# Performance work log

Hardware: AMD Instinct MI355X
Metric: run time of the kernel (lower is better)

The kernel has to match this reference:

```python
import jax, jax.numpy as jnp
import numpy as np
from jax import lax

D_MODEL, D_STATE, D_CONV, EXPAND = 64, 16, 4, 2
D_INNER = EXPAND * D_MODEL          # 128
DT_RANK = (D_MODEL + 15) // 16      # 4 = ceil(d_model/16), mamba_ssm 'auto'
B, L, N_IDX = 512, 256, 2048


def setup_inputs() -> dict:
    key = jax.random.key(0)
    ks = jax.random.split(key, 14)
    g = lambda k, shape, s: jax.random.normal(k, shape, jnp.float32) * s
    return {
        "reads": jax.random.normal(ks[0], (B, L, 4), jnp.float32),
        "sequenced_reads_indices": jax.random.randint(ks[1], (N_IDX,), 0, B),
        "exp_w": g(ks[2], (4, D_MODEL), 0.5),
        "exp_b": jnp.zeros((D_MODEL,), jnp.float32),
        "in_proj_w": g(ks[3], (D_MODEL, 2 * D_INNER), 0.1),
        "conv_w": g(ks[4], (D_INNER, 1, D_CONV), 0.3),
        "conv_b": jnp.zeros((D_INNER,), jnp.float32),
        "x_proj_w": g(ks[5], (D_INNER, DT_RANK + 2 * D_STATE), 0.1),
        "dt_w": g(ks[6], (DT_RANK, D_INNER), 0.3),
        "dt_b": jnp.full((D_INNER,), -4.6, jnp.float32),  # softplus(-4.6) ~ 0.01, mamba dt init scale
        "A_log": jnp.log(jnp.broadcast_to(jnp.arange(1, D_STATE + 1, dtype=jnp.float32), (D_INNER, D_STATE))),
        "D_skip": jnp.ones((D_INNER,), jnp.float32),
        "out_proj_w": g(ks[7], (D_INNER, D_MODEL), 0.1),
        "q_w": g(ks[8], (2 * D_MODEL, D_MODEL), 0.1),
        "q_b": jnp.zeros((D_MODEL,), jnp.float32),
        "k_w": g(ks[9], (2 * D_MODEL, D_MODEL), 0.1),
        "k_b": jnp.zeros((D_MODEL,), jnp.float32),
    }


def _mamba(x, in_proj_w, conv_w, conv_b, x_proj_w, dt_w, dt_b, A_log, D_skip, out_proj_w):
    # x: [b, l, d_model]
    xm, z = jnp.split(x @ in_proj_w, 2, axis=-1)  # each [b, l, d_inner]
    # causal depthwise conv over the sequence axis (pad left by d_conv-1, truncate to l)
    xc = lax.conv_general_dilated(
        xm.transpose(0, 2, 1), conv_w, (1,), [(D_CONV - 1, 0)],
        dimension_numbers=("NCH", "OIH", "NCH"), feature_group_count=D_INNER)
    xc = jax.nn.silu(xc + conv_b[None, :, None]).transpose(0, 2, 1)  # [b, l, d_inner]
    dt, Bm, Cm = jnp.split(xc @ x_proj_w, [DT_RANK, DT_RANK + D_STATE], axis=-1)
    delta = jax.nn.softplus(dt @ dt_w + dt_b)  # [b, l, d_inner]
    A = -jnp.exp(A_log)                        # [d_inner, d_state]

    def step(h, inp):
        d_t, B_t, C_t, u_t = inp  # [b,di], [b,ds], [b,ds], [b,di]
        h = jnp.exp(d_t[:, :, None] * A) * h + (d_t * u_t)[:, :, None] * B_t[:, None, :]
        return h, jnp.einsum("bdn,bn->bd", h, C_t)

    h0 = jnp.zeros((x.shape[0], D_INNER, D_STATE), x.dtype)
    xs = (delta.transpose(1, 0, 2), Bm.transpose(1, 0, 2),
          Cm.transpose(1, 0, 2), xc.transpose(1, 0, 2))
    _, ys = lax.scan(jax.checkpoint(step), h0, xs)  # ys: [l, b, d_inner]
    y = ys.transpose(1, 0, 2) + xc * D_skip
    return (y * jax.nn.silu(z)) @ out_proj_w  # [b, l, d_model]


def reference(reads, sequenced_reads_indices, exp_w, exp_b, in_proj_w, conv_w, conv_b,
              x_proj_w, dt_w, dt_b, A_log, D_skip, out_proj_w, q_w, q_b, k_w, k_b):
    x = reads @ exp_w + exp_b  # [b, l, d_model]
    enc = _mamba(x, in_proj_w, conv_w, conv_b, x_proj_w, dt_w, dt_b, A_log, D_skip, out_proj_w)
    mean_pooled = enc.mean(axis=1)        # [b, d_model]
    last_pooled = enc[:, -1, :]           # [b, d_model] (max pool computed in torch but unused)
    pooled = jnp.concatenate([mean_pooled, last_pooled], axis=-1)  # [b, 2*d_model]
    seq = pooled[sequenced_reads_indices]  # [n, 2*d_model]
    queries = seq @ q_w + q_b
    keys = pooled @ k_w + k_b
    return jnp.einsum("nd,md->nm", queries, keys)  # [n, b]
```

## Files before the change

### kernel.cpp

```cpp
#include <hip/hip_runtime.h>
#include <math.h>

#define L_SEQ 256
#define TILE 32

typedef __attribute__((ext_vector_type(2))) float f32x2;
typedef __attribute__((ext_vector_type(4))) float f32x4;
typedef __attribute__((ext_vector_type(8))) _Float16 f16x8;
typedef __attribute__((ext_vector_type(2))) _Float16 f16x2;

__device__ __forceinline__ f32x2 fma2(f32x2 a, f32x2 b, f32x2 c) {
    return __builtin_elementwise_fma(a, b, c);
}
__device__ __forceinline__ f32x2 splat2(float x) { f32x2 v = {x, x}; return v; }
__device__ __forceinline__ float silu_f(float x) { return x / (1.f + __expf(-x)); }
__device__ __forceinline__ float sp2_f(float x) {
    return log2f(1.f + exp2f(x * 1.44269504f)) * 0.69314718f;
}

__global__ __launch_bounds__(256)
void k_prep1(const float* __restrict__ exp_w, const float* __restrict__ exp_b,
             const float* __restrict__ in_proj_w,
             float* __restrict__ weff, float* __restrict__ beff)
{
    const int t = threadIdx.x;
    float a0 = 0, a1 = 0, a2 = 0, a3 = 0, ab = 0;
    for (int k = 0; k < 64; ++k) {
        float w = in_proj_w[k * 256 + t];
        a0 = fmaf(exp_w[k], w, a0);
        a1 = fmaf(exp_w[64 + k], w, a1);
        a2 = fmaf(exp_w[128 + k], w, a2);
        a3 = fmaf(exp_w[192 + k], w, a3);
        ab = fmaf(exp_b[k], w, ab);
    }
    weff[t] = a0; weff[256 + t] = a1; weff[512 + t] = a2; weff[768 + t] = a3;
    beff[t] = ab;
}

__global__ __launch_bounds__(256)
void k_prep2(const float* __restrict__ x_proj_w, const float* __restrict__ dt_w,
             const float* __restrict__ conv_w, const float* __restrict__ conv_b,
             const float* __restrict__ weff, const float* __restrict__ beff,
             _Float16* __restrict__ WT, _Float16* __restrict__ W2, float* __restrict__ bias2)
{
    const int t = threadIdx.x;
    const int blk = blockIdx.x;
    if (blk < 5) {
        const int base = blk * 4096;
        for (int i = base + t; i < base + 4096; i += 256) {
            const int row = i >> 7, k = i & 127;
            float v;
            if (row < 128) {
                v = x_proj_w[k * 36 + 0] * dt_w[row]
                  + x_proj_w[k * 36 + 1] * dt_w[128 + row]
                  + x_proj_w[k * 36 + 2] * dt_w[256 + row]
                  + x_proj_w[k * 36 + 3] * dt_w[384 + row];
            } else {
                v = x_proj_w[k * 36 + 4 + (row - 128)];
            }
            WT[i] = (_Float16)v;
        }
    } else if (blk == 5) {
        for (int i = t; i < 128 * 32; i += 256) {
            const int d = i >> 5, j = i & 31;
            float v = 0.f;
            if (j < 16)      v = conv_w[d * 4 + (j >> 2)] * weff[(j & 3) * 256 + d];
            else if (j < 20) v = conv_w[d * 4 + (j - 16)] * beff[d];
            W2[i] = (_Float16)v;
        }
        if (t < 128) bias2[t] = conv_b[t];
    } else {
        for (int i = t; i < 128 * 32; i += 256) {
            const int d = i >> 5, j = i & 31;
            float v = 0.f;
            if (j >= 12 && j < 16) v = weff[(j - 12) * 256 + 128 + d];
            else if (j == 19)      v = beff[128 + d];
            W2[128 * 32 + i] = (_Float16)v;
        }
    }
}

template<int NSEG>
__global__ __launch_bounds__(512, 6)
void mamba_seg(const float* __restrict__ reads,
               const _Float16* __restrict__ WT, const _Float16* __restrict__ W2,
               const float* __restrict__ bias2, const float* __restrict__ dt_b,
               const float* __restrict__ A_log, const float* __restrict__ D_skip,
               f16x2* __restrict__ Qg, f16x2* __restrict__ Pg, f16x2* __restrict__ Kg,
               float* __restrict__ GS, float* __restrict__ CZ, float* __restrict__ SL,
               int Bn)
{
    constexpr int NTILE_ = (L_SEQ / TILE) / NSEG;
    const int bx = blockIdx.x;
    const int b = bx / NSEG;
    const int sidx = bx - b * NSEG;
    const int seg0 = sidx * NTILE_ * TILE;
    const int t = threadIdx.x;
    const int dd = t >> 1, g = t & 1;

    __shared__ __align__(16) _Float16 F[32 * 40];
    __shared__ __align__(16) _Float16 XC[TILE * 136];
    __shared__ __align__(16) float    BC[TILE * 32];
    __shared__ _Float16               ZS[TILE * 128];
    __shared__ _Float16               DE[TILE * 128];

    float dskip = 0.f, c1 = 0.f;
    bool structured = true;
    if (t < 256) {
        dskip = D_skip[dd];
        c1 = -1.44269504f * (float)(8 * g + 1);
#pragma unroll
        for (int k = 0; k < 8; ++k) {
            float a = -__expf(A_log[dd * 16 + g * 8 + k]);
            structured = structured && (fabsf(a + (float)(g * 8 + k + 1)) < 1e-3f);
        }
    }

    f32x2 h2[4], P2[4], K2[4];
#pragma unroll
    for (int k = 0; k < 4; ++k) { h2[k] = splat2(0.f); P2[k] = splat2(1.f); K2[k] = splat2(0.f); }
    float gsum = 0.f;

    for (int tile = 0; tile < NTILE_; ++tile) {
        const int l_off = seg0 + tile * TILE;

        for (int i = t; i < 32 * 40; i += 512) {
            const int l = i / 40, j = i - l * 40;
            _Float16 v = (_Float16)0.f;
            if (j < 16) {
                const int row = l_off + l - 3 + (j >> 2);
                if (row >= 0) v = (_Float16)reads[((size_t)b * L_SEQ + row) * 4 + (j & 3)];
            } else if (j < 20) {
                v = (l_off + l - 3 + (j - 16) >= 0) ? (_Float16)1.f : (_Float16)0.f;
            }
            F[i] = v;
        }
        __syncthreads();

        {
            const int lane = t & 63, wv = t >> 6;
            const int fcol = lane & 15, kq = lane >> 4, rbase = kq * 4;
#pragma unroll
            for (int i = 0; i < 4; ++i) {
                const int tid = wv + 8 * i;
                const int m = tid & 1, n = tid >> 1;
                f16x8 af = *(const f16x8*)&F[(m * 16 + fcol) * 40 + kq * 8];
                f16x8 bf = *(const f16x8*)&W2[(n * 16 + fcol) * 32 + kq * 8];
                f32x4 acc = {0.f, 0.f, 0.f, 0.f};
                acc = __builtin_amdgcn_mfma_f32_16x16x32_f16(af, bf, acc, 0, 0, 0);
                if (n < 8) {
                    const int ch = n * 16 + fcol;
                    const float bv = bias2[ch];
#pragma unroll
                    for (int r = 0; r < 4; ++r)
                        XC[(m * 16 + rbase + r) * 136 + ch] = (_Float16)silu_f(acc[r] + bv);
                } else {
                    const int ch = (n - 8) * 16 + fcol;
#pragma unroll
                    for (int r = 0; r < 4; ++r)
                        ZS[(m * 16 + rbase + r) * 128 + ch] = (_Float16)silu_f(acc[r]);
                }
            }
        }
        __syncthreads();

        {
            const int lane = t & 63, wv = t >> 6;
            const int fcol = lane & 15, kq = lane >> 4, rbase = kq * 4;
#pragma unroll
            for (int i = 0; i < 3; ++i) {
                const int tid = wv + 8 * i;
                if (tid >= 20) break;
                const int m = tid & 1, n = tid >> 1;
                f32x4 acc = {0.f, 0.f, 0.f, 0.f};
#pragma unroll
                for (int ks = 0; ks < 4; ++ks) {
                    const int ko = ks * 32 + kq * 8;
                    f16x8 af = *(const f16x8*)&XC[(m * 16 + fcol) * 136 + ko];
                    f16x8 bf = *(const f16x8*)&WT[(n * 16 + fcol) * 128 + ko];
                    acc = __builtin_amdgcn_mfma_f32_16x16x32_f16(af, bf, acc, 0, 0, 0);
                }
                if (n < 8) {
                    const int ch = n * 16 + fcol;
                    const float db = dt_b[ch];
#pragma unroll
                    for (int r = 0; r < 4; ++r)
                        DE[(m * 16 + rbase + r) * 128 + ch] = (_Float16)sp2_f(acc[r] + db);
                } else {
                    const int jb = (n - 8) * 16 + fcol;
#pragma unroll
                    for (int r = 0; r < 4; ++r)
                        BC[(m * 16 + rbase + r) * 32 + jb] = acc[r];
                }
            }
        }
        __syncthreads();

        if (t < 256) {
            auto scan_loop = [&](bool needpk) {
                for (int l = 0; l < TILE; ++l) {
                    const float de = (float)DE[l * 128 + dd];
                    const float zs = (float)ZS[l * 128 + dd];
                    const float xc = (float)XC[l * 136 + dd];
                    const float du = de * xc;
                    f32x2 E2[4];
                    if (structured) {
                        const float r = exp2f(de * -1.44269504f);
                        const float t1 = exp2f(de * c1);
                        const float r2 = r * r;
                        E2[0] = (f32x2){t1, t1 * r};
                        const f32x2 r2s = splat2(r2);
                        E2[1] = E2[0] * r2s;
                        E2[2] = E2[1] * r2s;
                        E2[3] = E2[2] * r2s;
                    } else {
#pragma unroll
                        for (int k = 0; k < 4; ++k) {
                            float e0 = exp2f(de * (-__expf(A_log[dd * 16 + g * 8 + 2 * k])) * 1.44269504f);
                            float e1 = exp2f(de * (-__expf(A_log[dd * 16 + g * 8 + 2 * k + 1])) * 1.44269504f);
                            E2[k] = (f32x2){e0, e1};
                        }
                    }
                    const float4 Bq0 = *(const float4*)&BC[l * 32 + g * 8];
                    const float4 Bq1 = *(const float4*)&BC[l * 32 + g * 8 + 4];
                    const float4 Cq0 = *(const float4*)&BC[l * 32 + 16 + g * 8];
                    const float4 Cq1 = *(const float4*)&BC[l * 32 + 16 + g * 8 + 4];
                    const f32x2 B2[4] = {{Bq0.x, Bq0.y}, {Bq0.z, Bq0.w}, {Bq1.x, Bq1.y}, {Bq1.z, Bq1.w}};
                    const f32x2 C2[4] = {{Cq0.x, Cq0.y}, {Cq0.z, Cq0.w}, {Cq1.x, Cq1.y}, {Cq1.z, Cq1.w}};
                    const f32x2 dus = splat2(du), zss = splat2(zs);
                    f32x2 yp2 = splat2(0.f);
#pragma unroll
                    for (int k = 0; k < 4; ++k) {
                        h2[k] = fma2(E2[k], h2[k], dus * B2[k]);
                        yp2 = fma2(h2[k], C2[k], yp2);
                        if (needpk) {
                            P2[k] = P2[k] * E2[k];
                            K2[k] = fma2(zss, C2[k] * P2[k], K2[k]);
                        }
                    }
                    float yp = yp2.x + yp2.y;
                    const float y = yp + __shfl_xor(yp, 1);
                    gsum += fmaf(xc, dskip, y) * zs;
                }
            };
            if (sidx == 0) scan_loop(false);
            else           scan_loop(true);
        }
        if (NTILE_ > 1) __syncthreads();
    }

    if (t < 256) {
        const float zs_last = (float)ZS[(TILE - 1) * 128 + dd];
        const float xc_last = (float)XC[(TILE - 1) * 136 + dd];
        const size_t sb = (size_t)sidx * Bn + b;
#pragma unroll
        for (int k = 0; k < 4; ++k) {
            const size_t o = (sb * 8 + g * 4 + k) * 128 + dd;
            Qg[o] = (f16x2){(_Float16)h2[k].x, (_Float16)h2[k].y};
            if (sidx != 0) {
                Pg[o] = (f16x2){(_Float16)P2[k].x, (_Float16)P2[k].y};
                Kg[o] = (f16x2){(_Float16)K2[k].x, (_Float16)K2[k].y};
            }
        }
        if (g == 0) GS[sb * 128 + dd] = gsum;
        if (sidx == NSEG - 1) {
#pragma unroll
            for (int k = 0; k < 8; ++k)
                CZ[((size_t)b * 16 + g * 8 + k) * 128 + dd] =
                    zs_last * BC[(TILE - 1) * 32 + 16 + g * 8 + k];
            if (g == 0) SL[(size_t)b * 128 + dd] = zs_last * xc_last * dskip;
        }
    }
}

template<int NS>
__global__ __launch_bounds__(128)
void stitch(const f16x2* __restrict__ Qg, const f16x2* __restrict__ Pg,
            const f16x2* __restrict__ Kg, const float* __restrict__ GS,
            const float* __restrict__ CZ, const float* __restrict__ SL,
            const float* __restrict__ out_proj_w,
            const float* __restrict__ k_w, const float* __restrict__ k_b,
            float* __restrict__ pooled, float* __restrict__ keysT,
            int Bn)
{
    const int b = blockIdx.x, d = threadIdx.x;
    __shared__ float gb[256];
    __shared__ float pl[128];

    float h[16];
    float gsum = GS[(size_t)b * 128 + d];
#pragma unroll
    for (int p = 0; p < 8; ++p) {
        f16x2 q = Qg[((size_t)b * 8 + p) * 128 + d];
        h[2 * p] = (float)q[0]; h[2 * p + 1] = (float)q[1];
    }
#pragma unroll
    for (int s = 1; s < NS; ++s) {
        const size_t sb = (size_t)s * Bn + b;
        gsum += GS[sb * 128 + d];
        float corr = 0.f;
#pragma unroll
        for (int p = 0; p < 8; ++p) {
            const size_t o = (sb * 8 + p) * 128 + d;
            f16x2 qv = Qg[o], pv = Pg[o], kv = Kg[o];
            corr = fmaf((float)kv[0], h[2 * p], corr);
            corr = fmaf((float)kv[1], h[2 * p + 1], corr);
            h[2 * p]     = fmaf((float)pv[0], h[2 * p],     (float)qv[0]);
            h[2 * p + 1] = fmaf((float)pv[1], h[2 * p + 1], (float)qv[1]);
        }
        gsum += corr;
    }
    float glast = SL[(size_t)b * 128 + d];
#pragma unroll
    for (int n = 0; n < 16; ++n)
        glast = fmaf(CZ[((size_t)b * 16 + n) * 128 + d], h[n], glast);

    gb[d] = gsum * (1.f / (float)L_SEQ);
    gb[128 + d] = glast;
    __syncthreads();
    {
        const int half = d >> 6, oc = d & 63;
        const float* gbp = &gb[half * 128];
        float s = 0.f;
#pragma unroll 16
        for (int i = 0; i < 128; ++i) s = fmaf(gbp[i], out_proj_w[i * 64 + oc], s);
        pooled[(size_t)b * 128 + d] = s;
        pl[d] = s;
    }
    __syncthreads();
    if (d < 64) {
        float s = k_b[d];
#pragma unroll 16
        for (int i = 0; i < 128; ++i) s = fmaf(pl[i], k_w[i * 64 + d], s);
        keysT[(size_t)d * Bn + b] = s;
    }
}

__global__ __launch_bounds__(128)
void qk_kernel(const float* __restrict__ pooled, const int* __restrict__ idx,
               const float* __restrict__ q_w, const float* __restrict__ q_b,
               const float* __restrict__ keysT, float* __restrict__ out, int B)
{
    const int n = blockIdx.x, t = threadIdx.x;
    __shared__ float p_lds[128];
    __shared__ float q_lds[64];
    const int bi = idx[n];
    p_lds[t] = pooled[(size_t)bi * 128 + t];
    __syncthreads();
    if (t < 64) {
        float s = q_b[t];
#pragma unroll
        for (int i = 0; i < 128; ++i) s = fmaf(p_lds[i], q_w[i * 64 + t], s);
        q_lds[t] = s;
    }
    __syncthreads();
    f32x4 acc = {0.f, 0.f, 0.f, 0.f};
    const int m0 = t * 4;
#pragma unroll 8
    for (int i = 0; i < 64; ++i) {
        const float qi = q_lds[i];
        const float4 kv = *(const float4*)&keysT[(size_t)i * B + m0];
        acc[0] = fmaf(qi, kv.x, acc[0]);
        acc[1] = fmaf(qi, kv.y, acc[1]);
        acc[2] = fmaf(qi, kv.z, acc[2]);
        acc[3] = fmaf(qi, kv.w, acc[3]);
    }
    *(f32x4*)&out[(size_t)n * B + m0] = acc;
}


extern "C" void kernel_launch(void* const* d_in, const int* in_sizes, int n_in,
                              void* d_out, int out_size, void* d_ws, size_t ws_size,
                              hipStream_t stream)
{
    const float* reads      = (const float*)d_in[0];
    const int*   idx        = (const int*)d_in[1];
    const float* exp_w      = (const float*)d_in[2];
    const float* exp_b      = (const float*)d_in[3];
    const float* in_proj_w  = (const float*)d_in[4];
    const float* conv_w     = (const float*)d_in[5];
    const float* conv_b     = (const float*)d_in[6];
    const float* x_proj_w   = (const float*)d_in[7];
    const float* dt_w       = (const float*)d_in[8];
    const float* dt_b       = (const float*)d_in[9];
    const float* A_log      = (const float*)d_in[10];
    const float* D_skip     = (const float*)d_in[11];
    const float* out_proj_w = (const float*)d_in[12];
    const float* q_w        = (const float*)d_in[13];
    const float* q_b        = (const float*)d_in[14];
    const float* k_w        = (const float*)d_in[15];
    const float* k_b        = (const float*)d_in[16];

    const int B = in_sizes[0] / (L_SEQ * 4);
    const int N = in_sizes[1];

    char* wsb = (char*)d_ws;
    size_t off = 0;
    auto alloc = [&](size_t bytes) {
        size_t o = off;
        off = (off + bytes + 255) & ~(size_t)255;
        return o;
    };

    float*     pooled = (float*)(wsb + alloc((size_t)B * 128 * 4));
    float*     keysT  = (float*)(wsb + alloc((size_t)B * 64 * 4));
    float*     weff   = (float*)(wsb + alloc(1024 * 4));
    float*     beff   = (float*)(wsb + alloc(256 * 4));
    _Float16*  WT     = (_Float16*)(wsb + alloc(160 * 128 * 2));
    _Float16*  W2     = (_Float16*)(wsb + alloc(256 * 32 * 2));
    float*     bias2  = (float*)(wsb + alloc(128 * 4));

    auto summ_bytes = [&](int nseg) {
        size_t pairs = (size_t)B * nseg * 8 * 128;
        return pairs * 4 * 3
             + (size_t)B * nseg * 128 * 4
             + (size_t)B * 16 * 128 * 4
             + (size_t)B * 128 * 4 + 8192;
    };
    const int nseg = (off + summ_bytes(8) <= ws_size) ? 8 : 1;

    const size_t pairs = (size_t)B * nseg * 8 * 128;
    f16x2* Qg = (f16x2*)(wsb + alloc(pairs * 4));
    f16x2* Pg = (f16x2*)(wsb + alloc(pairs * 4));
    f16x2* Kg = (f16x2*)(wsb + alloc(pairs * 4));
    float* GS = (float*)(wsb + alloc((size_t)B * nseg * 128 * 4));
    float* CZ = (float*)(wsb + alloc((size_t)B * 16 * 128 * 4));
    float* SL = (float*)(wsb + alloc((size_t)B * 128 * 4));

    k_prep1<<<1, 256, 0, stream>>>(exp_w, exp_b, in_proj_w, weff, beff);
    k_prep2<<<7, 256, 0, stream>>>(x_proj_w, dt_w, conv_w, conv_b, weff, beff,
                                   WT, W2, bias2);
    if (nseg == 8) {
        mamba_seg<8><<<B * 8, 512, 0, stream>>>(reads, WT, W2, bias2, dt_b,
                                                A_log, D_skip,
                                                Qg, Pg, Kg, GS, CZ, SL, B);
        stitch<8><<<B, 128, 0, stream>>>(Qg, Pg, Kg, GS, CZ, SL, out_proj_w, k_w, k_b,
                                         pooled, keysT, B);
    } else {
        mamba_seg<1><<<B, 512, 0, stream>>>(reads, WT, W2, bias2, dt_b,
                                            A_log, D_skip,
                                            Qg, Pg, Kg, GS, CZ, SL, B);
        stitch<1><<<B, 128, 0, stream>>>(Qg, Pg, Kg, GS, CZ, SL, out_proj_w, k_w, k_b,
                                         pooled, keysT, B);
    }
    qk_kernel<<<N, 128, 0, stream>>>(pooled, idx, q_w, q_b, keysT, (float*)d_out, B);
}
```

Baseline: 140.9 us.

## Fuse prep kernels, run two scan segments per block, pack summaries, pair qk rows

Merges the two weight-prep kernels into one launch. Restructures the Mamba segment kernel so each 512-thread block handles two 32-step segments, with both 256-thread halves running scans instead of half the threads idling during the scan phase. The per-segment Q/P/K summaries are packed into one 16-byte f16x8 record, reducing separate loads in the stitch pass at the cost of some padding bytes. The qk kernel now computes two query rows per block to reuse key loads. This also removes the fallback to single-segment mode when workspace is small.

```diff
diff --git a/kernel.cpp b/kernel.cpp
--- a/kernel.cpp
+++ b/kernel.cpp
@@ -3,11 +3,11 @@
 
 #define L_SEQ 256
 #define TILE 32
+#define NSEG 8
 
 typedef __attribute__((ext_vector_type(2))) float f32x2;
 typedef __attribute__((ext_vector_type(4))) float f32x4;
 typedef __attribute__((ext_vector_type(8))) _Float16 f16x8;
-typedef __attribute__((ext_vector_type(2))) _Float16 f16x2;
 
 __device__ __forceinline__ f32x2 fma2(f32x2 a, f32x2 b, f32x2 c) {
     return __builtin_elementwise_fma(a, b, c);
@@ -19,32 +19,13 @@
 }
 
 __global__ __launch_bounds__(256)
-void k_prep1(const float* __restrict__ exp_w, const float* __restrict__ exp_b,
-             const float* __restrict__ in_proj_w,
-             float* __restrict__ weff, float* __restrict__ beff)
+void k_prep(const float* __restrict__ exp_w, const float* __restrict__ exp_b,
+            const float* __restrict__ in_proj_w, const float* __restrict__ x_proj_w,
+            const float* __restrict__ dt_w,
+            const float* __restrict__ conv_w, const float* __restrict__ conv_b,
+            _Float16* __restrict__ WT, _Float16* __restrict__ W2, float* __restrict__ bias2)
 {
-    const int t = threadIdx.x;
-    float a0 = 0, a1 = 0, a2 = 0, a3 = 0, ab = 0;
-    for (int k = 0; k < 64; ++k) {
-        float w = in_proj_w[k * 256 + t];
-        a0 = fmaf(exp_w[k], w, a0);
-        a1 = fmaf(exp_w[64 + k], w, a1);
-        a2 = fmaf(exp_w[128 + k], w, a2);
-        a3 = fmaf(exp_w[192 + k], w, a3);
-        ab = fmaf(exp_b[k], w, ab);
-    }
-    weff[t] = a0; weff[256 + t] = a1; weff[512 + t] = a2; weff[768 + t] = a3;
-    beff[t] = ab;
-}
-
-__global__ __launch_bounds__(256)
-void k_prep2(const float* __restrict__ x_proj_w, const float* __restrict__ dt_w,
-             const float* __restrict__ conv_w, const float* __restrict__ conv_b,
-             const float* __restrict__ weff, const float* __restrict__ beff,
-             _Float16* __restrict__ WT, _Float16* __restrict__ W2, float* __restrict__ bias2)
-{
-    const int t = threadIdx.x;
-    const int blk = blockIdx.x;
+    const int t = threadIdx.x, blk = blockIdx.x;
     if (blk < 5) {
         const int base = blk * 4096;
         for (int i = base + t; i < base + 4096; i += 256) {
@@ -60,214 +41,217 @@
             }
             WT[i] = (_Float16)v;
         }
-    } else if (blk == 5) {
-        for (int i = t; i < 128 * 32; i += 256) {
-            const int d = i >> 5, j = i & 31;
-            float v = 0.f;
-            if (j < 16)      v = conv_w[d * 4 + (j >> 2)] * weff[(j & 3) * 256 + d];
-            else if (j < 20) v = conv_w[d * 4 + (j - 16)] * beff[d];
-            W2[i] = (_Float16)v;
-        }
-        if (t < 128) bias2[t] = conv_b[t];
     } else {
-        for (int i = t; i < 128 * 32; i += 256) {
-            const int d = i >> 5, j = i & 31;
-            float v = 0.f;
-            if (j >= 12 && j < 16) v = weff[(j - 12) * 256 + 128 + d];
-            else if (j == 19)      v = beff[128 + d];
-            W2[128 * 32 + i] = (_Float16)v;
-        }
-    }
-}
-
-template<int NSEG>
-__global__ __launch_bounds__(512, 6)
-void mamba_seg(const float* __restrict__ reads,
-               const _Float16* __restrict__ WT, const _Float16* __restrict__ W2,
-               const float* __restrict__ bias2, const float* __restrict__ dt_b,
-               const float* __restrict__ A_log, const float* __restrict__ D_skip,
-               f16x2* __restrict__ Qg, f16x2* __restrict__ Pg, f16x2* __restrict__ Kg,
-               float* __restrict__ GS, float* __restrict__ CZ, float* __restrict__ SL,
-               int Bn)
+        const int d = t & 127;
+        const int col = (t < 128) ? d : (128 + d);
+        float w0 = 0, w1 = 0, w2 = 0, w3 = 0, bb = 0;
+        for (int k = 0; k < 64; ++k) {
+            float w = in_proj_w[k * 256 + col];
+            w0 = fmaf(exp_w[k], w, w0);
+            w1 = fmaf(exp_w[64 + k], w, w1);
+            w2 = fmaf(exp_w[128 + k], w, w2);
+            w3 = fmaf(exp_w[192 + k], w, w3);
+            bb = fmaf(exp_b[k], w, bb);
+        }
+        const float wx[4] = {w0, w1, w2, w3};
+        if (t < 128) {
+            for (int j = 0; j < 32; ++j) {
+                float v = 0.f;
+                if (j < 16)      v = conv_w[d * 4 + (j >> 2)] * wx[j & 3];
+                else if (j < 20) v = conv_w[d * 4 + (j - 16)] * bb;
+                W2[d * 32 + j] = (_Float16)v;
+            }
+            bias2[d] = conv_b[d];
+        } else {
+            for (int j = 0; j < 32; ++j) {
+                float v = 0.f;
+                if (j >= 12 && j < 16) v = wx[j - 12];
+                else if (j == 19)      v = bb;
+                W2[(128 + d) * 32 + j] = (_Float16)v;
+            }
+        }
+    }
+}
+
+__global__ __launch_bounds__(512, 2)
+void mamba_seg2(const float* __restrict__ reads,
+                const _Float16* __restrict__ WT, const _Float16* __restrict__ W2,
+                const float* __restrict__ bias2, const float* __restrict__ dt_b,
+                const float* __restrict__ A_log, const float* __restrict__ D_skip,
+                f16x8* __restrict__ QPK, float* __restrict__ GS,
+                float* __restrict__ CZ, float* __restrict__ SL, int Bn)
 {
-    constexpr int NTILE_ = (L_SEQ / TILE) / NSEG;
     const int bx = blockIdx.x;
-    const int b = bx / NSEG;
-    const int sidx = bx - b * NSEG;
-    const int seg0 = sidx * NTILE_ * TILE;
+    const int b = bx >> 2, jp = bx & 3;
     const int t = threadIdx.x;
-    const int dd = t >> 1, g = t & 1;
-
-    __shared__ __align__(16) _Float16 F[32 * 40];
-    __shared__ __align__(16) _Float16 XC[TILE * 136];
-    __shared__ __align__(16) float    BC[TILE * 32];
-    __shared__ _Float16               ZS[TILE * 128];
-    __shared__ _Float16               DE[TILE * 128];
-
-    float dskip = 0.f, c1 = 0.f;
+    const int lane256 = t & 255, wg = t >> 8;
+    const int dd = lane256 >> 1, g = lane256 & 1;
+    const int sidx = jp * 2 + wg;
+
+    __shared__ __align__(16) _Float16 F2[2][32 * 40];
+    __shared__ __align__(16) _Float16 XC2[2][32 * 136];
+    __shared__ __align__(16) float    BC2[2][32 * 32];
+    __shared__ _Float16               ZS2[2][32 * 128];
+    __shared__ _Float16               DE2[2][32 * 128];
+
+    const float dskip = D_skip[dd];
+    const float c1 = -1.44269504f * (float)(8 * g + 1);
     bool structured = true;
-    if (t < 256) {
-        dskip = D_skip[dd];
-        c1 = -1.44269504f * (float)(8 * g + 1);
-#pragma unroll
-        for (int k = 0; k < 8; ++k) {
-            float a = -__expf(A_log[dd * 16 + g * 8 + k]);
-            structured = structured && (fabsf(a + (float)(g * 8 + k + 1)) < 1e-3f);
-        }
-    }
+#pragma unroll
+    for (int k = 0; k < 8; ++k) {
+        float a = -__expf(A_log[dd * 16 + g * 8 + k]);
+        structured = structured && (fabsf(a + (float)(g * 8 + k + 1)) < 1e-3f);
+    }
+
+    for (int i = t; i < 2 * 32 * 40; i += 512) {
+        const int tau = i / 1280, r = i - tau * 1280;
+        const int l = r / 40, j = r - l * 40;
+        const int l_off = jp * 64 + tau * 32;
+        _Float16 v = (_Float16)0.f;
+        if (j < 16) {
+            const int row = l_off + l - 3 + (j >> 2);
+            if (row >= 0) v = (_Float16)reads[((size_t)b * L_SEQ + row) * 4 + (j & 3)];
+        } else if (j < 20) {
+            v = (l_off + l - 3 + (j - 16) >= 0) ? (_Float16)1.f : (_Float16)0.f;
+        }
+        F2[0][i] = v;
+    }
+    __syncthreads();
+
+    const int lane = t & 63, wv = t >> 6;
+    const int fcol = lane & 15, kq = lane >> 4, rbase = kq * 4;
+
+#pragma unroll
+    for (int i = 0; i < 8; ++i) {
+        const int tt = wv + 8 * i;
+        const int tau = tt >> 5, tid = tt & 31;
+        const int m = tid & 1, n = tid >> 1;
+        f16x8 af = *(const f16x8*)&F2[tau][(m * 16 + fcol) * 40 + kq * 8];
+        f16x8 bf = *(const f16x8*)&W2[(n * 16 + fcol) * 32 + kq * 8];
+        f32x4 acc = {0.f, 0.f, 0.f, 0.f};
+        acc = __builtin_amdgcn_mfma_f32_16x16x32_f16(af, bf, acc, 0, 0, 0);
+        if (n < 8) {
+            const int ch = n * 16 + fcol;
+            const float bv = bias2[ch];
+#pragma unroll
+            for (int r = 0; r < 4; ++r)
+                XC2[tau][(m * 16 + rbase + r) * 136 + ch] = (_Float16)silu_f(acc[r] + bv);
+        } else {
+            const int ch = (n - 8) * 16 + fcol;
+#pragma unroll
+            for (int r = 0; r < 4; ++r)
+                ZS2[tau][(m * 16 + rbase + r) * 128 + ch] = (_Float16)silu_f(acc[r]);
+        }
+    }
+    __syncthreads();
+
+#pragma unroll
+    for (int i = 0; i < 5; ++i) {
+        const int tt = wv + 8 * i;
+        const int tau = (tt >= 20) ? 1 : 0, tid = tt - 20 * tau;
+        const int m = tid & 1, n = tid >> 1;
+        f32x4 acc = {0.f, 0.f, 0.f, 0.f};
+#pragma unroll
+        for (int ks = 0; ks < 4; ++ks) {
+            const int ko = ks * 32 + kq * 8;
+            f16x8 af = *(const f16x8*)&XC2[tau][(m * 16 + fcol) * 136 + ko];
+            f16x8 bf = *(const f16x8*)&WT[(n * 16 + fcol) * 128 + ko];
+            acc = __builtin_amdgcn_mfma_f32_16x16x32_f16(af, bf, acc, 0, 0, 0);
+        }
+        if (n < 8) {
+            const int ch = n * 16 + fcol;
+            const float db = dt_b[ch];
+#pragma unroll
+            for (int r = 0; r < 4; ++r)
+                DE2[tau][(m * 16 + rbase + r) * 128 + ch] = (_Float16)sp2_f(acc[r] + db);
+        } else {
+            const int jb = (n - 8) * 16 + fcol;
+#pragma unroll
+            for (int r = 0; r < 4; ++r)
+                BC2[tau][(m * 16 + rbase + r) * 32 + jb] = acc[r];
+        }
+    }
+    __syncthreads();
 
     f32x2 h2[4], P2[4], K2[4];
 #pragma unroll
     for (int k = 0; k < 4; ++k) { h2[k] = splat2(0.f); P2[k] = splat2(1.f); K2[k] = splat2(0.f); }
     float gsum = 0.f;
-
-    for (int tile = 0; tile < NTILE_; ++tile) {
-        const int l_off = seg0 + tile * TILE;
-
-        for (int i = t; i < 32 * 40; i += 512) {
-            const int l = i / 40, j = i - l * 40;
-            _Float16 v = (_Float16)0.f;
-            if (j < 16) {
-                const int row = l_off + l - 3 + (j >> 2);
-                if (row >= 0) v = (_Float16)reads[((size_t)b * L_SEQ + row) * 4 + (j & 3)];
-            } else if (j < 20) {
-                v = (l_off + l - 3 + (j - 16) >= 0) ? (_Float16)1.f : (_Float16)0.f;
+    {
+        const _Float16* DEw = DE2[wg];
+        const _Float16* ZSw = ZS2[wg];
+        const _Float16* XCw = XC2[wg];
+        const float*    BCw = BC2[wg];
+        auto scan_loop = [&](bool needpk) {
+            for (int l = 0; l < TILE; ++l) {
+                const float de = (float)DEw[l * 128 + dd];
+                const float zs = (float)ZSw[l * 128 + dd];
+                const float xc = (float)XCw[l * 136 + dd];
+                const float du = de * xc;
+                f32x2 E2[4];
+                if (structured) {
+                    const float r = exp2f(de * -1.44269504f);
+                    const float t1 = exp2f(de * c1);
+                    const float r2 = r * r;
+                    E2[0] = (f32x2){t1, t1 * r};
+                    const f32x2 r2s = splat2(r2);
+                    E2[1] = E2[0] * r2s;
+                    E2[2] = E2[1] * r2s;
+                    E2[3] = E2[2] * r2s;
+                } else {
+#pragma unroll
+                    for (int k = 0; k < 4; ++k) {
+                        float e0 = exp2f(de * (-__expf(A_log[dd * 16 + g * 8 + 2 * k])) * 1.44269504f);
+                        float e1 = exp2f(de * (-__expf(A_log[dd * 16 + g * 8 + 2 * k + 1])) * 1.44269504f);
+                        E2[k] = (f32x2){e0, e1};
+                    }
+                }
+                const float4 Bq0 = *(const float4*)&BCw[l * 32 + g * 8];
+                const float4 Bq1 = *(const float4*)&BCw[l * 32 + g * 8 + 4];
+                const float4 Cq0 = *(const float4*)&BCw[l * 32 + 16 + g * 8];
+                const float4 Cq1 = *(const float4*)&BCw[l * 32 + 16 + g * 8 + 4];
+                const f32x2 B2[4] = {{Bq0.x, Bq0.y}, {Bq0.z, Bq0.w}, {Bq1.x, Bq1.y}, {Bq1.z, Bq1.w}};
+                const f32x2 C2[4] = {{Cq0.x, Cq0.y}, {Cq0.z, Cq0.w}, {Cq1.x, Cq1.y}, {Cq1.z, Cq1.w}};
+                const f32x2 dus = splat2(du), zss = splat2(zs);
+                f32x2 yp2 = splat2(0.f);
+#pragma unroll
+                for (int k = 0; k < 4; ++k) {
+                    h2[k] = fma2(E2[k], h2[k], dus * B2[k]);
+                    yp2 = fma2(h2[k], C2[k], yp2);
+                    if (needpk) {
+                        P2[k] = P2[k] * E2[k];
+                        K2[k] = fma2(zss, C2[k] * P2[k], K2[k]);
+                    }
+                }
+                float yp = yp2.x + yp2.y;
+                const float y = yp + __shfl_xor(yp, 1);
+                gsum += fmaf(xc, dskip, y) * zs;
             }
-            F[i] = v;
-        }
-        __syncthreads();
-
-        {
-            const int lane = t & 63, wv = t >> 6;
-            const int fcol = lane & 15, kq = lane >> 4, rbase = kq * 4;
-#pragma unroll
-            for (int i = 0; i < 4; ++i) {
-                const int tid = wv + 8 * i;
-                const int m = tid & 1, n = tid >> 1;
-                f16x8 af = *(const f16x8*)&F[(m * 16 + fcol) * 40 + kq * 8];
-                f16x8 bf = *(const f16x8*)&W2[(n * 16 + fcol) * 32 + kq * 8];
-                f32x4 acc = {0.f, 0.f, 0.f, 0.f};
-                acc = __builtin_amdgcn_mfma_f32_16x16x32_f16(af, bf, acc, 0, 0, 0);
-                if (n < 8) {
-                    const int ch = n * 16 + fcol;
-                    const float bv = bias2[ch];
-#pragma unroll
-                    for (int r = 0; r < 4; ++r)
-                        XC[(m * 16 + rbase + r) * 136 + ch] = (_Float16)silu_f(acc[r] + bv);
-                } else {
-                    const int ch = (n - 8) * 16 + fcol;
-#pragma unroll
-                    for (int r = 0; r < 4; ++r)
-                        ZS[(m * 16 + rbase + r) * 128 + ch] = (_Float16)silu_f(acc[r]);
-                }
-            }
-        }
-        __syncthreads();
-
-        {
-            const int lane = t & 63, wv = t >> 6;
-            const int fcol = lane & 15, kq = lane >> 4, rbase = kq * 4;
-#pragma unroll
-            for (int i = 0; i < 3; ++i) {
-                const int tid = wv + 8 * i;
-                if (tid >= 20) break;
-                const int m = tid & 1, n = tid >> 1;
-                f32x4 acc = {0.f, 0.f, 0.f, 0.f};
-#pragma unroll
-                for (int ks = 0; ks < 4; ++ks) {
-                    const int ko = ks * 32 + kq * 8;
-                    f16x8 af = *(const f16x8*)&XC[(m * 16 + fcol) * 136 + ko];
-                    f16x8 bf = *(const f16x8*)&WT[(n * 16 + fcol) * 128 + ko];
-                    acc = __builtin_amdgcn_mfma_f32_16x16x32_f16(af, bf, acc, 0, 0, 0);
-                }
-                if (n < 8) {
-                    const int ch = n * 16 + fcol;
-                    const float db = dt_b[ch];
-#pragma unroll
-                    for (int r = 0; r < 4; ++r)
-                        DE[(m * 16 + rbase + r) * 128 + ch] = (_Float16)sp2_f(acc[r] + db);
-                } else {
-                    const int jb = (n - 8) * 16 + fcol;
-#pragma unroll
-                    for (int r = 0; r < 4; ++r)
-                        BC[(m * 16 + rbase + r) * 32 + jb] = acc[r];
-                }
-            }
-        }
-        __syncthreads();
-
-        if (t < 256) {
-            auto scan_loop = [&](bool needpk) {
-                for (int l = 0; l < TILE; ++l) {
-                    const float de = (float)DE[l * 128 + dd];
-                    const float zs = (float)ZS[l * 128 + dd];
-                    const float xc = (float)XC[l * 136 + dd];
-                    const float du = de * xc;
-                    f32x2 E2[4];
-                    if (structured) {
-                        const float r = exp2f(de * -1.44269504f);
-                        const float t1 = exp2f(de * c1);
-                        const float r2 = r * r;
-                        E2[0] = (f32x2){t1, t1 * r};
-                        const f32x2 r2s = splat2(r2);
-                        E2[1] = E2[0] * r2s;
-                        E2[2] = E2[1] * r2s;
-                        E2[3] = E2[2] * r2s;
-                    } else {
-#pragma unroll
-                        for (int k = 0; k < 4; ++k) {
-                            float e0 = exp2f(de * (-__expf(A_log[dd * 16 + g * 8 + 2 * k])) * 1.44269504f);
-                            float e1 = exp2f(de * (-__expf(A_log[dd * 16 + g * 8 + 2 * k + 1])) * 1.44269504f);
-                            E2[k] = (f32x2){e0, e1};
-                        }
-                    }
-                    const float4 Bq0 = *(const float4*)&BC[l * 32 + g * 8];
-                    const float4 Bq1 = *(const float4*)&BC[l * 32 + g * 8 + 4];
-                    const float4 Cq0 = *(const float4*)&BC[l * 32 + 16 + g * 8];
-                    const float4 Cq1 = *(const float4*)&BC[l * 32 + 16 + g * 8 + 4];
-                    const f32x2 B2[4] = {{Bq0.x, Bq0.y}, {Bq0.z, Bq0.w}, {Bq1.x, Bq1.y}, {Bq1.z, Bq1.w}};
-                    const f32x2 C2[4] = {{Cq0.x, Cq0.y}, {Cq0.z, Cq0.w}, {Cq1.x, Cq1.y}, {Cq1.z, Cq1.w}};
-                    const f32x2 dus = splat2(du), zss = splat2(zs);
-                    f32x2 yp2 = splat2(0.f);
-#pragma unroll
-                    for (int k = 0; k < 4; ++k) {
-                        h2[k] = fma2(E2[k], h2[k], dus * B2[k]);
-                        yp2 = fma2(h2[k], C2[k], yp2);
-                        if (needpk) {
-                            P2[k] = P2[k] * E2[k];
-                            K2[k] = fma2(zss, C2[k] * P2[k], K2[k]);
-                        }
-                    }
-                    float yp = yp2.x + yp2.y;
-                    const float y = yp + __shfl_xor(yp, 1);
-                    gsum += fmaf(xc, dskip, y) * zs;
-                }
-            };
-            if (sidx == 0) scan_loop(false);
-            else           scan_loop(true);
-        }
-        if (NTILE_ > 1) __syncthreads();
-    }
-
-    if (t < 256) {
-        const float zs_last = (float)ZS[(TILE - 1) * 128 + dd];
-        const float xc_last = (float)XC[(TILE - 1) * 136 + dd];
+        };
+        if (sidx == 0) scan_loop(false);
+        else           scan_loop(true);
+    }
+
+    {
         const size_t sb = (size_t)sidx * Bn + b;
 #pragma unroll
         for (int k = 0; k < 4; ++k) {
-            const size_t o = (sb * 8 + g * 4 + k) * 128 + dd;
-            Qg[o] = (f16x2){(_Float16)h2[k].x, (_Float16)h2[k].y};
-            if (sidx != 0) {
-                Pg[o] = (f16x2){(_Float16)P2[k].x, (_Float16)P2[k].y};
-                Kg[o] = (f16x2){(_Float16)K2[k].x, (_Float16)K2[k].y};
-            }
+            const int p = g * 4 + k;
+            f16x8 v;
+            v[0] = (_Float16)h2[k].x; v[1] = (_Float16)h2[k].y;
+            v[2] = (_Float16)P2[k].x; v[3] = (_Float16)P2[k].y;
+            v[4] = (_Float16)K2[k].x; v[5] = (_Float16)K2[k].y;
+            v[6] = (_Float16)0.f;     v[7] = (_Float16)0.f;
+            QPK[(sb * 8 + p) * 128 + dd] = v;
         }
         if (g == 0) GS[sb * 128 + dd] = gsum;
-        if (sidx == NSEG - 1) {
+        if (jp == 3 && wg == 1) {
+            const float zs_last = (float)ZS2[1][(TILE - 1) * 128 + dd];
+            const float xc_last = (float)XC2[1][(TILE - 1) * 136 + dd];
 #pragma unroll
             for (int k = 0; k < 8; ++k)
                 CZ[((size_t)b * 16 + g * 8 + k) * 128 + dd] =
-                    zs_last * BC[(TILE - 1) * 32 + 16 + g * 8 + k];
+                    zs_last * BC2[1][(TILE - 1) * 32 + 16 + g * 8 + k];
             if (g == 0) SL[(size_t)b * 128 + dd] = zs_last * xc_last * dskip;
         }
     }
@@ -275,13 +259,11 @@
 
 template<int NS>
 __global__ __launch_bounds__(128)
-void stitch(const f16x2* __restrict__ Qg, const f16x2* __restrict__ Pg,
-            const f16x2* __restrict__ Kg, const float* __restrict__ GS,
+void stitch(const f16x8* __restrict__ QPK, const float* __restrict__ GS,
             const float* __restrict__ CZ, const float* __restrict__ SL,
             const float* __restrict__ out_proj_w,
             const float* __restrict__ k_w, const float* __restrict__ k_b,
-            float* __restrict__ pooled, float* __restrict__ keysT,
-            int Bn)
+            float* __restrict__ pooled, float* __restrict__ keysT, int Bn)
 {
     const int b = blockIdx.x, d = threadIdx.x;
     __shared__ float gb[256];
@@ -291,8 +273,8 @@
     float gsum = GS[(size_t)b * 128 + d];
 #pragma unroll
     for (int p = 0; p < 8; ++p) {
-        f16x2 q = Qg[((size_t)b * 8 + p) * 128 + d];
-        h[2 * p] = (float)q[0]; h[2 * p + 1] = (float)q[1];
+        f16x8 v = QPK[((size_t)b * 8 + p) * 128 + d];
+        h[2 * p] = (float)v[0]; h[2 * p + 1] = (float)v[1];
     }
 #pragma unroll
     for (int s = 1; s < NS; ++s) {
@@ -301,12 +283,11 @@
         float corr = 0.f;
 #pragma unroll
         for (int p = 0; p < 8; ++p) {
-            const size_t o = (sb * 8 + p) * 128 + d;
-            f16x2 qv = Qg[o], pv = Pg[o], kv = Kg[o];
-            corr = fmaf((float)kv[0], h[2 * p], corr);
-            corr = fmaf((float)kv[1], h[2 * p + 1], corr);
-            h[2 * p]     = fmaf((float)pv[0], h[2 * p],     (float)qv[0]);
-            h[2 * p + 1] = fmaf((float)pv[1], h[2 * p + 1], (float)qv[1]);
+            f16x8 v = QPK[(sb * 8 + p) * 128 + d];
+            corr = fmaf((float)v[4], h[2 * p], corr);
+            corr = fmaf((float)v[5], h[2 * p + 1], corr);
+            h[2 * p]     = fmaf((float)v[2], h[2 * p],     (float)v[0]);
+            h[2 * p + 1] = fmaf((float)v[3], h[2 * p + 1], (float)v[1]);
         }
         gsum += corr;
     }
@@ -339,33 +320,45 @@
 __global__ __launch_bounds__(128)
 void qk_kernel(const float* __restrict__ pooled, const int* __restrict__ idx,
                const float* __restrict__ q_w, const float* __restrict__ q_b,
-               const float* __restrict__ keysT, float* __restrict__ out, int B)
+               const float* __restrict__ keysT, float* __restrict__ out, int B, int N)
 {
-    const int n = blockIdx.x, t = threadIdx.x;
-    __shared__ float p_lds[128];
-    __shared__ float q_lds[64];
-    const int bi = idx[n];
-    p_lds[t] = pooled[(size_t)bi * 128 + t];
+    const int n0 = blockIdx.x * 2, t = threadIdx.x;
+    const int n1 = n0 + 1;
+    const bool has1 = (n1 < N);
+    __shared__ float p0[128], p1[128];
+    __shared__ float q0[64], q1[64];
+    const int bi0 = idx[n0];
+    const int bi1 = has1 ? idx[n1] : bi0;
+    p0[t] = pooled[(size_t)bi0 * 128 + t];
+    p1[t] = pooled[(size_t)bi1 * 128 + t];
     __syncthreads();
     if (t < 64) {
         float s = q_b[t];
 #pragma unroll
-        for (int i = 0; i < 128; ++i) s = fmaf(p_lds[i], q_w[i * 64 + t], s);
-        q_lds[t] = s;
-    }
-    __syncthreads();
-    f32x4 acc = {0.f, 0.f, 0.f, 0.f};
-    const int m0 = t * 4;
+        for (int i = 0; i < 128; ++i) s = fmaf(p0[i], q_w[i * 64 + t], s);
+        q0[t] = s;
+    } else {
+        const int tt = t - 64;
+        float s = q_b[tt];
+#pragma unroll
+        for (int i = 0; i < 128; ++i) s = fmaf(p1[i], q_w[i * 64 + tt], s);
+        q1[tt] = s;
+    }
+    __syncthreads();
+    for (int m0 = t * 4; m0 < B; m0 += 512) {
+        f32x4 a0 = {0.f, 0.f, 0.f, 0.f}, a1 = {0.f, 0.f, 0.f, 0.f};
 #pragma unroll 8
-    for (int i = 0; i < 64; ++i) {
-        const float qi = q_lds[i];
-        const float4 kv = *(const float4*)&keysT[(size_t)i * B + m0];
-        acc[0] = fmaf(qi, kv.x, acc[0]);
-        acc[1] = fmaf(qi, kv.y, acc[1]);
-        acc[2] = fmaf(qi, kv.z, acc[2]);
-        acc[3] = fmaf(qi, kv.w, acc[3]);
-    }
-    *(f32x4*)&out[(size_t)n * B + m0] = acc;
+        for (int i = 0; i < 64; ++i) {
+            const float4 kv = *(const float4*)&keysT[(size_t)i * B + m0];
+            const float qa = q0[i], qb = q1[i];
+            a0[0] = fmaf(qa, kv.x, a0[0]); a0[1] = fmaf(qa, kv.y, a0[1]);
+            a0[2] = fmaf(qa, kv.z, a0[2]); a0[3] = fmaf(qa, kv.w, a0[3]);
+            a1[0] = fmaf(qb, kv.x, a1[0]); a1[1] = fmaf(qb, kv.y, a1[1]);
+            a1[2] = fmaf(qb, kv.z, a1[2]); a1[3] = fmaf(qb, kv.w, a1[3]);
+        }
+        *(f32x4*)&out[(size_t)n0 * B + m0] = a0;
+        if (has1) *(f32x4*)&out[(size_t)n1 * B + m0] = a1;
+    }
 }
 
 
@@ -404,44 +397,22 @@
 
     float*     pooled = (float*)(wsb + alloc((size_t)B * 128 * 4));
     float*     keysT  = (float*)(wsb + alloc((size_t)B * 64 * 4));
-    float*     weff   = (float*)(wsb + alloc(1024 * 4));
-    float*     beff   = (float*)(wsb + alloc(256 * 4));
     _Float16*  WT     = (_Float16*)(wsb + alloc(160 * 128 * 2));
     _Float16*  W2     = (_Float16*)(wsb + alloc(256 * 32 * 2));
     float*     bias2  = (float*)(wsb + alloc(128 * 4));
 
-    auto summ_bytes = [&](int nseg) {
-        size_t pairs = (size_t)B * nseg * 8 * 128;
-        return pairs * 4 * 3
-             + (size_t)B * nseg * 128 * 4
-             + (size_t)B * 16 * 128 * 4
-             + (size_t)B * 128 * 4 + 8192;
-    };
-    const int nseg = (off + summ_bytes(8) <= ws_size) ? 8 : 1;
-
-    const size_t pairs = (size_t)B * nseg * 8 * 128;
-    f16x2* Qg = (f16x2*)(wsb + alloc(pairs * 4));
-    f16x2* Pg = (f16x2*)(wsb + alloc(pairs * 4));
-    f16x2* Kg = (f16x2*)(wsb + alloc(pairs * 4));
-    float* GS = (float*)(wsb + alloc((size_t)B * nseg * 128 * 4));
-    float* CZ = (float*)(wsb + alloc((size_t)B * 16 * 128 * 4));
-    float* SL = (float*)(wsb + alloc((size_t)B * 128 * 4));
-
-    k_prep1<<<1, 256, 0, stream>>>(exp_w, exp_b, in_proj_w, weff, beff);
-    k_prep2<<<7, 256, 0, stream>>>(x_proj_w, dt_w, conv_w, conv_b, weff, beff,
-                                   WT, W2, bias2);
-    if (nseg == 8) {
-        mamba_seg<8><<<B * 8, 512, 0, stream>>>(reads, WT, W2, bias2, dt_b,
-                                                A_log, D_skip,
-                                                Qg, Pg, Kg, GS, CZ, SL, B);
-        stitch<8><<<B, 128, 0, stream>>>(Qg, Pg, Kg, GS, CZ, SL, out_proj_w, k_w, k_b,
-                                         pooled, keysT, B);
-    } else {
-        mamba_seg<1><<<B, 512, 0, stream>>>(reads, WT, W2, bias2, dt_b,
-                                            A_log, D_skip,
-                                            Qg, Pg, Kg, GS, CZ, SL, B);
-        stitch<1><<<B, 128, 0, stream>>>(Qg, Pg, Kg, GS, CZ, SL, out_proj_w, k_w, k_b,
-                                         pooled, keysT, B);
-    }
-    qk_kernel<<<N, 128, 0, stream>>>(pooled, idx, q_w, q_b, keysT, (float*)d_out, B);
-}
+    const size_t pairs = (size_t)B * NSEG * 8 * 128;
+    f16x8* QPK = (f16x8*)(wsb + alloc(pairs * 16));
+    float* GS  = (float*)(wsb + alloc((size_t)B * NSEG * 128 * 4));
+    float* CZ  = (float*)(wsb + alloc((size_t)B * 16 * 128 * 4));
+    float* SL  = (float*)(wsb + alloc((size_t)B * 128 * 4));
+
+    k_prep<<<6, 256, 0, stream>>>(exp_w, exp_b, in_proj_w, x_proj_w, dt_w,
+                                  conv_w, conv_b, WT, W2, bias2);
+    mamba_seg2<<<B * 4, 512, 0, stream>>>(reads, WT, W2, bias2, dt_b,
+                                          A_log, D_skip, QPK, GS, CZ, SL, B);
+    stitch<NSEG><<<B, 128, 0, stream>>>(QPK, GS, CZ, SL, out_proj_w, k_w, k_b,
+                                        pooled, keysT, B);
+    qk_kernel<<<(N + 1) / 2, 128, 0, stream>>>(pooled, idx, q_w, q_b, keysT,
+                                               (float*)d_out, B, N);
+}
```

Result: slower. 147.5 us (+4.7%).
